# Kernel tuning notes

Hardware: AMD Instinct MI355X
Metric: run time of the kernel (lower is better)

Reference implementation:

```python
import jax, jax.numpy as jnp
import numpy as np

N = 10000      # nodes
E = 160000     # edges
F_IN = 84
H = 256
P = 4          # powers [0,1,2,3]
L = 3          # mixhop layers


def setup_inputs() -> dict:
    key = jax.random.key(0)
    ks = jax.random.split(key, 10)
    s = 0.05
    inp = {}
    inp["x"] = jax.random.normal(ks[0], (N, F_IN), jnp.float32)
    inp["edge_index"] = jax.random.randint(ks[1], (2, E), 0, N, dtype=jnp.int32)
    inp["w_in"] = jax.random.normal(ks[2], (F_IN, H), jnp.float32) * s
    inp["b_in"] = jnp.zeros((H,), jnp.float32)
    inp["mh_w0"] = jax.random.normal(ks[3], (P, H, H), jnp.float32) * s
    inp["mh_b0"] = jnp.zeros((P, H), jnp.float32)
    inp["mh_w12"] = jax.random.normal(ks[4], (2, P, P * H, H), jnp.float32) * s
    inp["mh_b12"] = jnp.zeros((2, P, H), jnp.float32)
    inp["ln_g"] = jnp.ones((L, P * H), jnp.float32)
    inp["ln_b"] = jnp.zeros((L, P * H), jnp.float32)
    inp["w1"] = jax.random.normal(ks[5], (P * H, H), jnp.float32) * s
    inp["b1"] = jnp.zeros((H,), jnp.float32)
    inp["w2"] = jax.random.normal(ks[6], (H, H // 2), jnp.float32) * s
    inp["b2"] = jnp.zeros((H // 2,), jnp.float32)
    inp["w3"] = jax.random.normal(ks[7], (H // 2, 1), jnp.float32) * s
    inp["b3"] = jnp.zeros((1,), jnp.float32)
    return inp


def _gcn_norm(edge_index, n):
    # D^{-1/2} (A + I) D^{-1/2}, PyG gcn_norm with add_self_loops=True
    loop = jnp.arange(n, dtype=edge_index.dtype)
    src = jnp.concatenate([edge_index[0], loop])
    dst = jnp.concatenate([edge_index[1], loop])
    deg = jax.ops.segment_sum(jnp.ones(src.shape[0], jnp.float32), dst, num_segments=n)
    dinv = jnp.where(deg > 0, deg ** -0.5, 0.0)
    return src, dst, dinv[src] * dinv[dst]


def _propagate(h, src, dst, w, n):
    # out[i] = sum_{(j->i)} w_e * h[j]
    return jax.ops.segment_sum(h[src] * w[:, None], dst, num_segments=n)


def _mixhop(h, src, dst, w, n, W, B):
    outs = [h @ W[0] + B[0]]  # power 0
    for p in range(1, W.shape[0]):
        h = _propagate(h, src, dst, w, n)
        outs.append(h @ W[p] + B[p])
    return jnp.concatenate(outs, axis=-1)  # [n, P*H]


def _layernorm(x, g, b, eps=1e-5):
    mu = x.mean(-1, keepdims=True)
    var = x.var(-1, keepdims=True)
    return (x - mu) * jax.lax.rsqrt(var + eps) * g + b


def reference(x, edge_index, w_in, b_in, mh_w0, mh_b0, mh_w12, mh_b12,
              ln_g, ln_b, w1, b1, w2, b2, w3, b3):
    gelu = lambda t: jax.nn.gelu(t, approximate=False)  # torch default (erf)
    n = x.shape[0]
    src, dst, w = _gcn_norm(edge_index, n)
    h = gelu(x @ w_in + b_in)
    for i in range(L):
        W, B = (mh_w0, mh_b0) if i == 0 else (mh_w12[i - 1], mh_b12[i - 1])
        h = _mixhop(h, src, dst, w, n, W, B)
        h = gelu(_layernorm(h, ln_g[i], ln_b[i]))
        # dropout inactive at inference
    h = gelu(h @ w1 + b1)
    h = gelu(h @ w2 + b2)
    out = h @ w3 + b3
    return out.squeeze(-1)  # [N]
```

## Files before the change

### kernel.cpp

```cpp
#include <hip/hip_runtime.h>

typedef unsigned short u16;
typedef unsigned int u32;
typedef __bf16 bf16x8 __attribute__((ext_vector_type(8)));
typedef float f32x4 __attribute__((ext_vector_type(4)));

#define NN 10000
#define EE 160000
#define MPAD 10112

__device__ inline float b2f(u16 u) { return __uint_as_float(((u32)u) << 16); }
__device__ inline u16 f2b(float f) {
    u32 u = __float_as_uint(f);
    return (u16)((u + 0x7fffu + ((u >> 16) & 1u)) >> 16);
}
__device__ inline float gelu_f(float x) {
    return 0.5f * x * (1.0f + erff(x * 0.70710678118654752f));
}
__device__ inline void load_lds16(const u16* g, u16* l) {
    __builtin_amdgcn_global_load_lds((const __attribute__((address_space(1))) u32*)g,
                                     (__attribute__((address_space(3))) u32*)l, 16, 0, 0);
}

__global__ __launch_bounds__(256) void k_count(const int* __restrict__ dst, int* __restrict__ cnt) {
    int e = blockIdx.x * 256 + threadIdx.x;
    if (e < EE) atomicAdd(&cnt[dst[e]], 1);
}

__global__ __launch_bounds__(256) void k_scan(const int* __restrict__ cnt, int* __restrict__ rowptr,
                                              int* __restrict__ cursor, float* __restrict__ dinv) {
    __shared__ int part[256];
    const int t = threadIdx.x;
    const int CH = 40;
    int base = t * CH;
    int ssum = 0;
    for (int k = 0; k < CH; k++) { int i = base + k; if (i < NN) ssum += cnt[i]; }
    part[t] = ssum;
    __syncthreads();
    for (int off = 1; off < 256; off <<= 1) {
        int v = (t >= off) ? part[t - off] : 0;
        __syncthreads();
        part[t] += v;
        __syncthreads();
    }
    int run = part[t] - ssum;
    for (int k = 0; k < CH; k++) {
        int i = base + k;
        if (i < NN) {
            rowptr[i] = run; cursor[i] = run;
            int c = cnt[i];
            dinv[i] = rsqrtf((float)(c + 1));
            run += c;
        }
    }
    if (t == 255) rowptr[NN] = run;
}

__global__ __launch_bounds__(256) void k_fill(const int* __restrict__ src, const int* __restrict__ dst,
                                              int* __restrict__ cursor, int* __restrict__ cols,
                                              float* __restrict__ vals, const float* __restrict__ dinv) {
    int e = blockIdx.x * 256 + threadIdx.x;
    if (e < EE) {
        int s = src[e], d = dst[e];
        int pos = atomicAdd(&cursor[d], 1);
        cols[pos] = s;
        vals[pos] = dinv[s] * dinv[d];
    }
}

__global__ __launch_bounds__(256) void k_padx(const float* __restrict__ x, u16* __restrict__ xp) {
    int idx = blockIdx.x * 256 + threadIdx.x;
    if (idx >= MPAD * 96) return;
    int r = idx / 96, c = idx - r * 96;
    u16 v = 0;
    if (r < NN && c < 84) v = f2b(x[(size_t)r * 84 + c]);
    xp[idx] = v;
}

struct TT { const float* src; u16* dst; int K, Nc, Kp; };
__global__ __launch_bounds__(256) void k_transT(TT t0, TT t1, TT t2, TT t3, TT t4) {
    int b = blockIdx.x; TT T;
    if (b < 8)        { T = t0; }
    else if (b < 72)  { T = t1; b -= 8; }
    else if (b < 584) { T = t2; b -= 72; }
    else if (b < 648) { T = t3; b -= 584; }
    else              { T = t4; b -= 648; }
    int tk = (T.K + 63) >> 6, tn = T.Nc >> 6;
    int bb  = b / (tk * tn);
    int rem = b - bb * (tk * tn);
    int k0 = (rem / tn) * 64, n0 = (rem % tn) * 64;
    __shared__ u16 tile[64][65];
    const float* src = T.src + (size_t)bb * T.K * T.Nc;
    u16* dst = T.dst + (size_t)bb * T.Nc * T.Kp;
    int c = threadIdx.x & 63, r0 = threadIdx.x >> 6;
#pragma unroll
    for (int i = 0; i < 16; i++) {
        int r = r0 + i * 4;
        int k = k0 + r;
        u16 v = 0;
        if (k < T.K) v = f2b(src[(size_t)k * T.Nc + n0 + c]);
        tile[r][c] = v;
    }
    __syncthreads();
    int rr = threadIdx.x & 63, cc0 = threadIdx.x >> 6;
#pragma unroll
    for (int i = 0; i < 16; i++) {
        int cc = cc0 + i * 4;
        int k = k0 + rr;
        if (k < T.Kp) dst[(size_t)(n0 + cc) * T.Kp + k] = tile[rr][cc];
    }
}

struct CvtSrcs { const float *b_in, *mh_b0, *mh_b12, *ln_g, *ln_b, *b1, *b2, *w3, *b3; };
__global__ __launch_bounds__(256) void k_cvt_all(CvtSrcs S, u16* __restrict__ dst) {
    int i = blockIdx.x * 256 + threadIdx.x;
    const float* s; int base;
    if (i < 256)       { s = S.b_in;   base = 0; }
    else if (i < 1280) { s = S.mh_b0;  base = 256; }
    else if (i < 3328) { s = S.mh_b12; base = 1280; }
    else if (i < 6400) { s = S.ln_g;   base = 3328; }
    else if (i < 9472) { s = S.ln_b;   base = 6400; }
    else if (i < 9728) { s = S.b1;     base = 9472; }
    else if (i < 9856) { s = S.b2;     base = 9728; }
    else if (i < 9984) { s = S.w3;     base = 9856; }
    else if (i < 9985) { s = S.b3;     base = 9984; }
    else return;
    dst[i] = f2b(s[i - base]);
}

template<int TM, int TN, int ACT, int EPI, int BATCH>
__global__ __launch_bounds__(256) void k_gemm(const u16* __restrict__ A0, const u16* __restrict__ A1,
                                              const u16* __restrict__ A2, const u16* __restrict__ A3,
                                              const u16* __restrict__ Bt, const u16* __restrict__ bias,
                                              u16* __restrict__ C, u16* __restrict__ Z,
                                              int K, int ldc, int col0, int NB_M, int NB_N) {
    constexpr int AM = TM / 32, AN = TN / 32;
    constexpr int CA = TM / 16, CB = TN / 16;
    constexpr int NCH = (CA + CB) / 4;
    __shared__ __align__(16) u16 As[TM * 32];
    __shared__ __align__(16) u16 Bs[TN * 32];
    int id = blockIdx.x;
    int g8 = id & 7, sIdx = id >> 3;
    int nb = sIdx % NB_N, jb = sIdx / NB_N;
    int mb = g8 + 8 * jb;
    if (mb >= NB_M) return;
    const u16* A = A0;
    if (BATCH) {
        int z = blockIdx.y;
        if (z == 1) A = A1; else if (z == 2) A = A2; else if (z == 3) A = A3;
        Bt   += (size_t)z * 256 * K;
        bias += z * 256;
        col0 += z * 256;
    }
    const int t = threadIdx.x;
    const int wv = t >> 6, lane = t & 63;
    const int wm = wv >> 1, wn = wv & 1;
    const int quad = lane >> 4, l16 = lane & 15;
    const int tileM = mb * TM, tileN = nb * TN;

    f32x4 acc[AM][AN] = {};

    const int rch = lane >> 2, c8 = (lane & 3) * 8;
    const u16* gsrc[NCH];
    u16* ldst[NCH];
#pragma unroll
    for (int i = 0; i < NCH; i++) {
        int c = wv + 4 * i;
        if (c < CA) {
            gsrc[i] = A + (size_t)(tileM + c * 16 + rch) * K + c8;
            ldst[i] = &As[c * 512 + lane * 8];
        } else {
            int cc = c - CA;
            gsrc[i] = Bt + (size_t)(tileN + cc * 16 + rch) * K + c8;
            ldst[i] = &Bs[cc * 512 + lane * 8];
        }
    }

    for (int k0 = 0; k0 < K; k0 += 32) {
        __syncthreads();
#pragma unroll
        for (int i = 0; i < NCH; i++) load_lds16(gsrc[i] + k0, ldst[i]);
        __syncthreads();
        bf16x8 af[AM], bfr[AN];
#pragma unroll
        for (int tm = 0; tm < AM; tm++)
            af[tm] = *(const bf16x8*)&As[(wm * (TM / 2) + tm * 16 + l16) * 32 + quad * 8];
#pragma unroll
        for (int tn = 0; tn < AN; tn++)
            bfr[tn] = *(const bf16x8*)&Bs[(wn * (TN / 2) + tn * 16 + l16) * 32 + quad * 8];
#pragma unroll
        for (int tm = 0; tm < AM; tm++)
#pragma unroll
            for (int tn = 0; tn < AN; tn++)
                acc[tm][tn] = __builtin_amdgcn_mfma_f32_16x16x32_bf16(af[tm], bfr[tn], acc[tm][tn], 0, 0, 0);
    }

#pragma unroll
    for (int tm = 0; tm < AM; tm++)
#pragma unroll
        for (int tn = 0; tn < AN; tn++)
#pragma unroll
            for (int r = 0; r < 4; r++) {
                int row = tileM + wm * (TM / 2) + tm * 16 + quad * 4 + r;
                int col = tileN + wn * (TN / 2) + tn * 16 + l16;
                float v = acc[tm][tn][r];
                if (EPI == 2) {
                    if (col < 256) C[(size_t)row * 1024 + col] = f2b(v + b2f(bias[col]));
                    else           Z[(size_t)row * 768 + (col - 256)] = f2b(v);
                } else {
                    v += b2f(bias[col]);
                    if (ACT) v = gelu_f(v);
                    C[(size_t)row * ldc + col0 + col] = f2b(v);
                }
            }
}

template<int CAT0>
__global__ __launch_bounds__(256) void k_propw(const u16* __restrict__ hin, int W, int G,
                                               const int* __restrict__ rowptr, const int* __restrict__ cols,
                                               const float* __restrict__ vals, const float* __restrict__ dinv,
                                               u16* __restrict__ concat, const u16* __restrict__ bias,
                                               int col0, u16* __restrict__ out2) {
    int unit = blockIdx.x * 4 + (threadIdx.x >> 6);
    if (unit >= NN * G) return;
    int node = unit / G, g = unit - node * G;
    int lane = threadIdx.x & 63;
    int half = lane >> 5, fl = lane & 31;
    const u16* base = hin + g * 256 + fl * 8;
    float a0 = 0, a1 = 0, a2 = 0, a3 = 0, a4 = 0, a5 = 0, a6 = 0, a7 = 0;
    if (half == 1) {
        float di = dinv[node], sw = di * di;
        bf16x8 sv = *(const bf16x8*)(base + (size_t)node * W);
        a0 = sw * (float)sv[0]; a1 = sw * (float)sv[1]; a2 = sw * (float)sv[2]; a3 = sw * (float)sv[3];
        a4 = sw * (float)sv[4]; a5 = sw * (float)sv[5]; a6 = sw * (float)sv[6]; a7 = sw * (float)sv[7];
    }
    int s = rowptr[node], e = rowptr[node + 1];
    int q = s + half;
    for (; q + 2 < e; q += 4) {
        int j0 = cols[q],  j1 = cols[q + 2];
        float w0 = vals[q], w1 = vals[q + 2];
        bf16x8 v0 = *(const bf16x8*)(base + (size_t)j0 * W);
        bf16x8 v1 = *(const bf16x8*)(base + (size_t)j1 * W);
        a0 += w0 * (float)v0[0] + w1 * (float)v1[0];
        a1 += w0 * (float)v0[1] + w1 * (float)v1[1];
        a2 += w0 * (float)v0[2] + w1 * (float)v1[2];
        a3 += w0 * (float)v0[3] + w1 * (float)v1[3];
        a4 += w0 * (float)v0[4] + w1 * (float)v1[4];
        a5 += w0 * (float)v0[5] + w1 * (float)v1[5];
        a6 += w0 * (float)v0[6] + w1 * (float)v1[6];
        a7 += w0 * (float)v0[7] + w1 * (float)v1[7];
    }
    if (q < e) {
        int j = cols[q];
        float w = vals[q];
        bf16x8 v = *(const bf16x8*)(base + (size_t)j * W);
        a0 += w * (float)v[0]; a1 += w * (float)v[1]; a2 += w * (float)v[2]; a3 += w * (float)v[3];
        a4 += w * (float)v[4]; a5 += w * (float)v[5]; a6 += w * (float)v[6]; a7 += w * (float)v[7];
    }
    a0 += __shfl_down(a0, 32); a1 += __shfl_down(a1, 32);
    a2 += __shfl_down(a2, 32); a3 += __shfl_down(a3, 32);
    a4 += __shfl_down(a4, 32); a5 += __shfl_down(a5, 32);
    a6 += __shfl_down(a6, 32); a7 += __shfl_down(a7, 32);
    if (half == 0) {
        int f = fl * 8;
        union { u16 u[8]; uint4 v; } pk;
        if (CAT0 && g == 0) {
            pk.u[0] = f2b(a0 + b2f(bias[f + 0])); pk.u[1] = f2b(a1 + b2f(bias[f + 1]));
            pk.u[2] = f2b(a2 + b2f(bias[f + 2])); pk.u[3] = f2b(a3 + b2f(bias[f + 3]));
            pk.u[4] = f2b(a4 + b2f(bias[f + 4])); pk.u[5] = f2b(a5 + b2f(bias[f + 5]));
            pk.u[6] = f2b(a6 + b2f(bias[f + 6])); pk.u[7] = f2b(a7 + b2f(bias[f + 7]));
            *(uint4*)(concat + (size_t)node * 1024 + col0 + f) = pk.v;
        } else {
            int W2 = W - CAT0 * 256;
            pk.u[0] = f2b(a0); pk.u[1] = f2b(a1); pk.u[2] = f2b(a2); pk.u[3] = f2b(a3);
            pk.u[4] = f2b(a4); pk.u[5] = f2b(a5); pk.u[6] = f2b(a6); pk.u[7] = f2b(a7);
            *(uint4*)(out2 + (size_t)node * W2 + (g - CAT0) * 256 + f) = pk.v;
        }
    }
}

__global__ __launch_bounds__(256) void k_ln_gelu(const u16* __restrict__ X, const u16* __restrict__ g,
                                                 const u16* __restrict__ b, u16* __restrict__ out) {
    __shared__ float red[256];
    const int row = blockIdx.x, t = threadIdx.x;
    ushort4 xv = *(const ushort4*)(X + (size_t)row * 1024 + t * 4);
    float x0 = b2f(xv.x), x1 = b2f(xv.y), x2 = b2f(xv.z), x3 = b2f(xv.w);
    red[t] = x0 + x1 + x2 + x3;
    __syncthreads();
    for (int off = 128; off; off >>= 1) {
        if (t < off) red[t] += red[t + off];
        __syncthreads();
    }
    float mu = red[0] * (1.f / 1024.f);
    __syncthreads();
    float d0 = x0 - mu, d1 = x1 - mu, d2 = x2 - mu, d3 = x3 - mu;
    red[t] = d0 * d0 + d1 * d1 + d2 * d2 + d3 * d3;
    __syncthreads();
    for (int off = 128; off; off >>= 1) {
        if (t < off) red[t] += red[t + off];
        __syncthreads();
    }
    float rs = rsqrtf(red[0] * (1.f / 1024.f) + 1e-5f);
    int c = t * 4;
    ushort4 gv = *(const ushort4*)(g + c);
    ushort4 bv = *(const ushort4*)(b + c);
    ushort4 o;
    o.x = f2b(gelu_f(d0 * rs * b2f(gv.x) + b2f(bv.x)));
    o.y = f2b(gelu_f(d1 * rs * b2f(gv.y) + b2f(bv.y)));
    o.z = f2b(gelu_f(d2 * rs * b2f(gv.z) + b2f(bv.z)));
    o.w = f2b(gelu_f(d3 * rs * b2f(gv.w) + b2f(bv.w)));
    *(ushort4*)(out + (size_t)row * 1024 + c) = o;
}

__global__ __launch_bounds__(256) void k_final(const u16* __restrict__ h, const u16* __restrict__ w3,
                                               const u16* __restrict__ b3, float* __restrict__ out) {
    int gw = (blockIdx.x * 256 + threadIdx.x) >> 6;
    int lane = threadIdx.x & 63;
    if (gw >= NN) return;
    u32 hv = *(const u32*)(h + (size_t)gw * 128 + lane * 2);
    u32 wv = *(const u32*)(w3 + lane * 2);
    float s = b2f((u16)(hv & 0xffff)) * b2f((u16)(wv & 0xffff)) +
              b2f((u16)(hv >> 16)) * b2f((u16)(wv >> 16));
    for (int off = 32; off; off >>= 1) s += __shfl_down(s, off);
    if (lane == 0) out[gw] = s + b2f(b3[0]);
}

extern "C" void kernel_launch(void* const* d_in, const int* in_sizes, int n_in,
                              void* d_out, int out_size, void* d_ws, size_t ws_size,
                              hipStream_t stream) {
    (void)in_sizes; (void)n_in; (void)out_size; (void)ws_size;
    const float* x  = (const float*)d_in[0];
    const int*   ei = (const int*)d_in[1];
    float* out = (float*)d_out;

    char* p = (char*)d_ws;
    auto alloc = [&](size_t bytes) { char* q = p; p += (bytes + 255) & ~(size_t)255; return q; };
    int*   cnt    = (int*)alloc(NN * 4);
    int*   rowptr = (int*)alloc((NN + 1) * 4);
    int*   cursor = (int*)alloc(NN * 4);
    float* dinv   = (float*)alloc(NN * 4);
    int*   cols   = (int*)alloc(EE * 4);
    float* vals   = (float*)alloc(EE * 4);
    u16*   xp     = (u16*)alloc((size_t)MPAD * 96 * 2);
    u16*   wbuf   = (u16*)alloc((size_t)2678784 * 2);
    u16*   smallC = (u16*)alloc(10240 * 2);
    u16*   S1     = (u16*)alloc((size_t)MPAD * 256 * 2);
    u16*   S2     = (u16*)alloc((size_t)MPAD * 256 * 2);
    u16*   S3     = (u16*)alloc((size_t)MPAD * 256 * 2);
    u16*   S4     = (u16*)alloc((size_t)MPAD * 256 * 2);
    u16*   Zb     = (u16*)alloc((size_t)MPAD * 768 * 2);
    u16*   Y2     = (u16*)alloc((size_t)MPAD * 512 * 2);
    u16*   Y3     = (u16*)alloc((size_t)MPAD * 256 * 2);
    u16*   bufA   = (u16*)alloc((size_t)MPAD * 1024 * 2);
    u16*   concat = (u16*)alloc((size_t)MPAD * 1024 * 2);

    u16* winT  = wbuf;
    u16* w0T   = wbuf + 24576;
    u16* w12T  = wbuf + 286720;
    u16* w1T   = wbuf + 2383872;
    u16* w2T   = wbuf + 2646016;
    u16* binC  = smallC;
    u16* mb0C  = smallC + 256;
    u16* mb12C = smallC + 1280;
    u16* lngC  = smallC + 3328;
    u16* lnbC  = smallC + 6400;
    u16* b1C   = smallC + 9472;
    u16* b2C   = smallC + 9728;
    u16* w3C   = smallC + 9856;
    u16* b3C   = smallC + 9984;

    const int* srcA = ei;
    const int* dstA = ei + EE;

    hipMemsetAsync(cnt, 0, NN * 4, stream);

    k_padx<<<(MPAD * 96 + 255) / 256, 256, 0, stream>>>(x, xp);
    TT t0{(const float*)d_in[2],  winT, 84,   256, 96};
    TT t1{(const float*)d_in[4],  w0T,  256,  256, 256};
    TT t2{(const float*)d_in[6],  w12T, 1024, 256, 1024};
    TT t3{(const float*)d_in[10], w1T,  1024, 256, 1024};
    TT t4{(const float*)d_in[12], w2T,  256,  128, 256};
    k_transT<<<656, 256, 0, stream>>>(t0, t1, t2, t3, t4);
    CvtSrcs CS{(const float*)d_in[3], (const float*)d_in[5], (const float*)d_in[7],
               (const float*)d_in[8], (const float*)d_in[9], (const float*)d_in[11],
               (const float*)d_in[13], (const float*)d_in[14], (const float*)d_in[15]};
    k_cvt_all<<<40, 256, 0, stream>>>(CS, smallC);

    k_count<<<(EE + 255) / 256, 256, 0, stream>>>(dstA, cnt);
    k_scan<<<1, 256, 0, stream>>>(cnt, rowptr, cursor, dinv);
    k_fill<<<(EE + 255) / 256, 256, 0, stream>>>(srcA, dstA, cursor, cols, vals, dinv);

    auto gx = [](int nbm, int nbn) { return 8 * ((nbm + 7) / 8) * nbn; };

    k_gemm<128, 64, 1, 0, 0><<<gx(79, 4), 256, 0, stream>>>(xp, xp, xp, xp, winT, binC, S1, nullptr, 96, 256, 0, 79, 4);

    k_propw<0><<<2500, 256, 0, stream>>>(S1, 256, 1, rowptr, cols, vals, dinv, nullptr, nullptr, 0, S2);
    k_propw<0><<<2500, 256, 0, stream>>>(S2, 256, 1, rowptr, cols, vals, dinv, nullptr, nullptr, 0, S3);
    k_propw<0><<<2500, 256, 0, stream>>>(S3, 256, 1, rowptr, cols, vals, dinv, nullptr, nullptr, 0, S4);
    k_gemm<128, 64, 0, 0, 1><<<dim3(gx(79, 4), 4), 256, 0, stream>>>(S1, S2, S3, S4, w0T, mb0C, concat, nullptr, 256, 1024, 0, 79, 4);
    k_ln_gelu<<<NN, 256, 0, stream>>>(concat, lngC, lnbC, bufA);

    for (int L = 0; L < 2; L++) {
        const u16* WT = w12T + (size_t)L * 1024 * 1024;
        const u16* BB = mb12C + L * 1024;
        k_gemm<128, 64, 0, 2, 0><<<gx(79, 16), 256, 0, stream>>>(bufA, bufA, bufA, bufA, WT, BB, concat, Zb, 1024, 0, 0, 79, 16);
        k_propw<1><<<7500, 256, 0, stream>>>(Zb, 768, 3, rowptr, cols, vals, dinv, concat, BB + 256, 256, Y2);
        k_propw<1><<<5000, 256, 0, stream>>>(Y2, 512, 2, rowptr, cols, vals, dinv, concat, BB + 512, 512, Y3);
        k_propw<1><<<2500, 256, 0, stream>>>(Y3, 256, 1, rowptr, cols, vals, dinv, concat, BB + 768, 768, Y3);
        k_ln_gelu<<<NN, 256, 0, stream>>>(concat, lngC + (L + 1) * 1024, lnbC + (L + 1) * 1024, bufA);
    }

    k_gemm<64, 64, 1, 0, 0><<<gx(158, 4), 256, 0, stream>>>(bufA, bufA, bufA, bufA, w1T, b1C, S1, nullptr, 1024, 256, 0, 158, 4);
    k_gemm<64, 64, 1, 0, 0><<<gx(158, 2), 256, 0, stream>>>(S1, S1, S1, S1, w2T, b2C, S2, nullptr, 256, 128, 0, 158, 2);
    k_final<<<2500, 256, 0, stream>>>(S2, w3C, b3C, out);
}
```

Baseline: 519.8 us.

## Double-buffer GEMM LDS tiles and unroll SpMM gather loop by four

The GEMM kernel now keeps two LDS buffers for the A and B tiles. It prefetches the next K-slice with global_load_lds while MFMA runs on the current slice, and needs one barrier per iteration instead of two. The sparse propagation kernel gains a 4-way unrolled edge loop, so more independent neighbour-row loads are in flight per lane. The cost is doubled LDS per block, which may reduce occupancy, plus higher register pressure in the gather loop.

Measured after the change: 505.2 us. 2.8% less time.

```diff
diff --git a/kernel.cpp b/kernel.cpp
--- a/kernel.cpp
+++ b/kernel.cpp
@@ -137,8 +137,8 @@
     constexpr int AM = TM / 32, AN = TN / 32;
     constexpr int CA = TM / 16, CB = TN / 16;
     constexpr int NCH = (CA + CB) / 4;
-    __shared__ __align__(16) u16 As[TM * 32];
-    __shared__ __align__(16) u16 Bs[TN * 32];
+    __shared__ __align__(16) u16 As[2][TM * 32];
+    __shared__ __align__(16) u16 Bs[2][TN * 32];
     int id = blockIdx.x;
     int g8 = id & 7, sIdx = id >> 3;
     int nb = sIdx % NB_N, jb = sIdx / NB_N;
@@ -162,32 +162,42 @@
 
     const int rch = lane >> 2, c8 = (lane & 3) * 8;
     const u16* gsrc[NCH];
-    u16* ldst[NCH];
+    u16* l0[NCH]; u16* l1[NCH];
 #pragma unroll
     for (int i = 0; i < NCH; i++) {
         int c = wv + 4 * i;
         if (c < CA) {
             gsrc[i] = A + (size_t)(tileM + c * 16 + rch) * K + c8;
-            ldst[i] = &As[c * 512 + lane * 8];
+            l0[i] = &As[0][c * 512 + lane * 8];
+            l1[i] = &As[1][c * 512 + lane * 8];
         } else {
             int cc = c - CA;
             gsrc[i] = Bt + (size_t)(tileN + cc * 16 + rch) * K + c8;
-            ldst[i] = &Bs[cc * 512 + lane * 8];
+            l0[i] = &Bs[0][cc * 512 + lane * 8];
+            l1[i] = &Bs[1][cc * 512 + lane * 8];
         }
     }
 
-    for (int k0 = 0; k0 < K; k0 += 32) {
+#pragma unroll
+    for (int i = 0; i < NCH; i++) load_lds16(gsrc[i], l0[i]);
+
+    int kb = 0;
+    for (int k0 = 0; k0 < K; k0 += 32, kb ^= 1) {
         __syncthreads();
-#pragma unroll
-        for (int i = 0; i < NCH; i++) load_lds16(gsrc[i] + k0, ldst[i]);
-        __syncthreads();
+        if (k0 + 32 < K) {
+#pragma unroll
+            for (int i = 0; i < NCH; i++)
+                load_lds16(gsrc[i] + k0 + 32, kb ? l0[i] : l1[i]);
+        }
+        const u16* Ab = As[kb];
+        const u16* Bb = Bs[kb];
         bf16x8 af[AM], bfr[AN];
 #pragma unroll
         for (int tm = 0; tm < AM; tm++)
-            af[tm] = *(const bf16x8*)&As[(wm * (TM / 2) + tm * 16 + l16) * 32 + quad * 8];
+            af[tm] = *(const bf16x8*)&Ab[(wm * (TM / 2) + tm * 16 + l16) * 32 + quad * 8];
 #pragma unroll
         for (int tn = 0; tn < AN; tn++)
-            bfr[tn] = *(const bf16x8*)&Bs[(wn * (TN / 2) + tn * 16 + l16) * 32 + quad * 8];
+            bfr[tn] = *(const bf16x8*)&Bb[(wn * (TN / 2) + tn * 16 + l16) * 32 + quad * 8];
 #pragma unroll
         for (int tm = 0; tm < AM; tm++)
 #pragma unroll
@@ -236,8 +246,24 @@
     }
     int s = rowptr[node], e = rowptr[node + 1];
     int q = s + half;
+    for (; q + 6 < e; q += 8) {
+        int j0 = cols[q], j1 = cols[q + 2], j2 = cols[q + 4], j3 = cols[q + 6];
+        float w0 = vals[q], w1 = vals[q + 2], w2 = vals[q + 4], w3 = vals[q + 6];
+        bf16x8 v0 = *(const bf16x8*)(base + (size_t)j0 * W);
+        bf16x8 v1 = *(const bf16x8*)(base + (size_t)j1 * W);
+        bf16x8 v2 = *(const bf16x8*)(base + (size_t)j2 * W);
+        bf16x8 v3 = *(const bf16x8*)(base + (size_t)j3 * W);
+        a0 += w0 * (float)v0[0] + w1 * (float)v1[0] + w2 * (float)v2[0] + w3 * (float)v3[0];
+        a1 += w0 * (float)v0[1] + w1 * (float)v1[1] + w2 * (float)v2[1] + w3 * (float)v3[1];
+        a2 += w0 * (float)v0[2] + w1 * (float)v1[2] + w2 * (float)v2[2] + w3 * (float)v3[2];
+        a3 += w0 * (float)v0[3] + w1 * (float)v1[3] + w2 * (float)v2[3] + w3 * (float)v3[3];
+        a4 += w0 * (float)v0[4] + w1 * (float)v1[4] + w2 * (float)v2[4] + w3 * (float)v3[4];
+        a5 += w0 * (float)v0[5] + w1 * (float)v1[5] + w2 * (float)v2[5] + w3 * (float)v3[5];
+        a6 += w0 * (float)v0[6] + w1 * (float)v1[6] + w2 * (float)v2[6] + w3 * (float)v3[6];
+        a7 += w0 * (float)v0[7] + w1 * (float)v1[7] + w2 * (float)v2[7] + w3 * (float)v3[7];
+    }
     for (; q + 2 < e; q += 4) {
-        int j0 = cols[q],  j1 = cols[q + 2];
+        int j0 = cols[q], j1 = cols[q + 2];
         float w0 = vals[q], w1 = vals[q + 2];
         bf16x8 v0 = *(const bf16x8*)(base + (size_t)j0 * W);
         bf16x8 v1 = *(const bf16x8*)(base + (size_t)j1 * W);
```
